# Performance work log

Hardware: AMD Instinct MI355X
Metric: run time of the kernel (lower is better)

The kernel has to match this reference:

```python
import jax, jax.numpy as jnp
import numpy as np

ALPHA = 0.99  # EMA decay used in ewa_func


def setup_inputs() -> dict:
    key = jax.random.key(0)
    k1, k2 = jax.random.split(key)
    N, K, D = 65536, 2048, 128  # flattened latents, vq_num, vq_dim
    initrange = 1.0 / D  # matches init_embed uniform_(-1/vq_dim, 1/vq_dim)
    return {
        "Z": jax.random.normal(k1, (N, D), dtype=jnp.float32),
        "dict_val": jax.random.uniform(k2, (K, D), dtype=jnp.float32,
                                       minval=-initrange, maxval=initrange),
        "dict_cnt": jnp.ones((K,), dtype=jnp.float32),
    }


def reference(Z, dict_val, dict_cnt):
    K, D = dict_val.shape
    # pairwise squared L2 dist: ((Z[:,None]-W[None,:])**2).sum(2), computed as
    # ||z||^2 - 2 z.w + ||w||^2 (same math, GEMM-efficient form)
    z2 = jnp.sum(Z * Z, axis=1)                      # [N]
    w2 = jnp.sum(dict_val * dict_val, axis=1)        # [K]
    dist = z2[:, None] - 2.0 * (Z @ dict_val.T) + w2[None, :]  # [N, K]
    i = jnp.argmin(dist, axis=1)                     # [N] assigned codes

    # EMA codebook update, only for clusters that received assignments
    counts = jax.ops.segment_sum(jnp.ones((Z.shape[0],), Z.dtype), i, num_segments=K)  # [K]
    sums = jax.ops.segment_sum(Z, i, num_segments=K)  # [K, D]
    assigned = counts > 0
    c_new = jnp.where(assigned, ALPHA * dict_cnt + (1.0 - ALPHA) * counts, dict_cnt)
    w_new = jnp.where(
        assigned[:, None],
        ALPHA * dict_val + (1.0 - ALPHA) * sums / jnp.maximum(c_new, 1e-12)[:, None],
        dict_val,
    )

    W_j = w_new[i]                                   # [N, D] quantized vectors
    # straight-through estimator: forward = W_j (detached), grad passes to Z
    st_out = Z + jax.lax.stop_gradient(W_j - Z)
    # commit_loss = L2_dist(Z, sg(W_j)).sum(1).mean()
    diff = Z - jax.lax.stop_gradient(W_j)
    commit_loss = jnp.mean(jnp.sum(diff * diff, axis=1))
    return st_out, commit_loss, w_new, c_new
```

## Files before the change

kernel.cpp:

```cpp
#include <hip/hip_runtime.h>
#include <hip/hip_bf16.h>

#define NN 65536
#define KK 2048
#define DD 128

typedef __attribute__((ext_vector_type(8))) _Float16 f16x8;
typedef __attribute__((ext_vector_type(16))) float f32x16;

static __device__ __forceinline__ unsigned encf(float f) {
    unsigned u = __float_as_uint(f);
    return u ^ (((unsigned)((int)u >> 31)) | 0x80000000u);
}

static __device__ __forceinline__ void gll16(const void* g, void* l) {
    __builtin_amdgcn_global_load_lds(
        (const __attribute__((address_space(1))) void*)g,
        (__attribute__((address_space(3))) void*)l, 16, 0, 0);
}

__global__ __launch_bounds__(256) void vq_prep(const float* __restrict__ Wd,
                                               _Float16* __restrict__ Wre,
                                               float* __restrict__ w2)
{
    int tid = threadIdx.x;
    int rl = tid >> 4, c = tid & 15;
    int r = blockIdx.x * 16 + rl;
    const float4* wp = reinterpret_cast<const float4*>(Wd + (size_t)r * DD + c * 8);
    float4 v0 = wp[0], v1 = wp[1];
    float v[8] = {v0.x, v0.y, v0.z, v0.w, v1.x, v1.y, v1.z, v1.w};

    f16x8 hv;
#pragma unroll
    for (int j = 0; j < 8; ++j) hv[j] = (_Float16)(v[j] * 128.0f);

    float p = 0.f;
#pragma unroll
    for (int j = 0; j < 8; ++j) p = fmaf(v[j], v[j], p);
#pragma unroll
    for (int off2 = 1; off2 < 16; off2 <<= 1) p += __shfl_xor(p, off2, 64);

    int t = c >> 1, g = c & 1;
    size_t off = (size_t)(r >> 7) * 16384 + (size_t)((r >> 5) & 3) * 4096
               + t * 512 + g * 256 + (size_t)(r & 31) * 8;
    *reinterpret_cast<f16x8*>(Wre + off) = hv;
    if (c == 0) w2[r] = p;
}

__global__ __launch_bounds__(256, 2) void vq_gemm(const float* __restrict__ Z,
                                                  const _Float16* __restrict__ Wre,
                                                  const float* __restrict__ w2g,
                                                  const float* __restrict__ Wd,
                                                  int* __restrict__ assign,
                                                  float* __restrict__ counts)
{
    int rb  = blockIdx.x;
    int tid = threadIdx.x;
    int wid = tid >> 6, lane = tid & 63;
    int g2 = lane >> 5, l31 = lane & 31;

    __shared__ _Float16 Bs[2][16384];
    __shared__ float W2s[2048];
    __shared__ float2 T2s[128];

#pragma unroll
    for (int j = 0; j < 2; ++j)
        gll16(w2g + j * 1024 + tid * 4, &W2s[j * 1024 + tid * 4]);
#pragma unroll
    for (int j = 0; j < 8; ++j)
        gll16(Wre + j * 2048 + tid * 8, &Bs[0][j * 2048 + tid * 8]);

    const float* zrow = Z + ((size_t)(rb * 128 + wid * 32 + l31)) * DD + g2 * 8;
    f16x8 a[8];
#pragma unroll
    for (int t = 0; t < 8; ++t) {
        float4 u0 = *reinterpret_cast<const float4*>(zrow + t * 16);
        float4 u1 = *reinterpret_cast<const float4*>(zrow + t * 16 + 4);
        f16x8 h;
        h[0] = (_Float16)u0.x; h[1] = (_Float16)u0.y;
        h[2] = (_Float16)u0.z; h[3] = (_Float16)u0.w;
        h[4] = (_Float16)u1.x; h[5] = (_Float16)u1.y;
        h[6] = (_Float16)u1.z; h[7] = (_Float16)u1.w;
        a[t] = h;
    }

    const float INF = __uint_as_float(0x7F800000u);
    float t1[16], t2[16];
#pragma unroll
    for (int s = 0; s < 16; ++s) { t1[s] = INF; t2[s] = INF; }

    const f32x16 zz = {};

    int cur = 0;
#pragma unroll 1
    for (int it = 0; it < 16; ++it) {
        if (it < 15) {
            const _Float16* wb = Wre + (size_t)(it + 1) * 16384;
#pragma unroll
            for (int j = 0; j < 8; ++j)
                gll16(wb + j * 2048 + tid * 8, &Bs[cur ^ 1][j * 2048 + tid * 8]);
            asm volatile("s_waitcnt vmcnt(8)" ::: "memory");
        } else {
            asm volatile("s_waitcnt vmcnt(0)" ::: "memory");
        }
        __builtin_amdgcn_s_barrier();

        float w2v[4];
#pragma unroll
        for (int ct = 0; ct < 4; ++ct) w2v[ct] = W2s[it * 128 + ct * 32 + l31];

        const _Float16* bb = &Bs[cur][g2 * 256 + l31 * 8];
        f32x16 acc[4];
        __builtin_amdgcn_s_setprio(1);
#pragma unroll
        for (int ct = 0; ct < 4; ++ct) {
#pragma unroll
            for (int t = 0; t < 8; ++t) {
                f16x8 b = *reinterpret_cast<const f16x8*>(bb + ct * 4096 + t * 512);
                acc[ct] = __builtin_amdgcn_mfma_f32_32x32x16_f16(
                    a[t], b, (t == 0) ? zz : acc[ct], 0, 0, 0);
            }
        }
        __builtin_amdgcn_s_setprio(0);

#pragma unroll
        for (int ct = 0; ct < 4; ++ct) {
            unsigned ci = (unsigned)(it * 128 + ct * 32 + l31);
#pragma unroll
            for (int r = 0; r < 16; ++r) {
                float d = fmaf(-0.015625f, acc[ct][r], w2v[ct]);
                float df = __uint_as_float((__float_as_uint(d) & 0xFFFFF800u) | ci);
                t2[r] = __builtin_amdgcn_fmed3f(df, t1[r], t2[r]);
                t1[r] = fminf(t1[r], df);
            }
        }

        __builtin_amdgcn_s_barrier();
        cur ^= 1;
    }

#pragma unroll
    for (int s = 0; s < 16; ++s) {
        float v1 = t1[s], v2 = t2[s];
#pragma unroll
        for (int msk = 1; msk < 32; msk <<= 1) {
            float o1 = __shfl_xor(v1, msk, 64);
            float o2 = __shfl_xor(v2, msk, 64);
            float mx = fmaxf(v1, o1);
            v1 = fminf(v1, o1);
            v2 = fminf(fminf(v2, o2), mx);
        }
        if (l31 == 0) {
            int rl = wid * 32 + (s & 3) + 8 * (s >> 2) + 4 * g2;
            T2s[rl] = make_float2(v1, v2);
        }
    }
    __syncthreads();

    if (tid < 128) {
        int row = rb * 128 + tid;
        float2 t2v = T2s[tid];
        unsigned u1 = __float_as_uint(t2v.x);
        unsigned u2 = __float_as_uint(t2v.y);
        int c1 = (int)(u1 & 2047u), c2 = (int)(u2 & 2047u);
        float d1 = __uint_as_float(u1 & 0xFFFFF800u);
        float d2 = __uint_as_float(u2 & 0xFFFFF800u);

        int res = c1;
        if (d2 - d1 <= 1e-3f) {
            int cols[2] = {c1, c2};
            const float4* zp = reinterpret_cast<const float4*>(Z + (size_t)row * DD);
            float s0 = 0.f, s1 = 0.f, s2 = 0.f, s3 = 0.f;
            for (int q = 0; q < 32; ++q) {
                float4 z = zp[q];
                s0 = fmaf(z.x, z.x, s0);
                s1 = fmaf(z.y, z.y, s1);
                s2 = fmaf(z.z, z.z, s2);
                s3 = fmaf(z.w, z.w, s3);
            }
            float z2v = (s0 + s1) + (s2 + s3);
            unsigned long long be = ~0ull;
            for (int i = 0; i < 2; ++i) {
                int k = cols[i];
                const float4* wp = reinterpret_cast<const float4*>(Wd + (size_t)k * DD);
                float a0 = 0.f, a1 = 0.f, a2 = 0.f, a3 = 0.f;
                for (int q = 0; q < 32; ++q) {
                    float4 zq = zp[q];
                    float4 wq = wp[q];
                    a0 = fmaf(zq.x, wq.x, a0);
                    a1 = fmaf(zq.y, wq.y, a1);
                    a2 = fmaf(zq.z, wq.z, a2);
                    a3 = fmaf(zq.w, wq.w, a3);
                }
                float sdot = (a0 + a1) + (a2 + a3);
                float tt = __fsub_rn(z2v, __fmul_rn(2.0f, sdot));
                float dist = __fadd_rn(tt, W2s[k]);
                unsigned long long key =
                    (((unsigned long long)encf(dist)) << 32) | (unsigned)k;
                if (key < be) be = key;
            }
            res = (int)(be & 0xffffffffu);
        }
        assign[row] = res;
        atomicAdd(&counts[res], 1.0f);
    }
}

__global__ __launch_bounds__(256) void vq_scan(const float* __restrict__ counts,
                                               int* __restrict__ start,
                                               int* __restrict__ cursor)
{
    __shared__ int ps[256];
    int tid = threadIdx.x;
    int c[8];
    int tot = 0;
#pragma unroll
    for (int j = 0; j < 8; ++j) { c[j] = (int)counts[tid * 8 + j]; tot += c[j]; }
    ps[tid] = tot;
    __syncthreads();
    for (int off = 1; off < 256; off <<= 1) {
        int v = (tid >= off) ? ps[tid - off] : 0;
        __syncthreads();
        ps[tid] += v;
        __syncthreads();
    }
    int base = ps[tid] - tot;
#pragma unroll
    for (int j = 0; j < 8; ++j) {
        start[tid * 8 + j] = base;
        cursor[tid * 8 + j] = base;
        base += c[j];
    }
}

__global__ __launch_bounds__(256) void vq_permute(const int* __restrict__ assign,
                                                  int* __restrict__ cursor,
                                                  int* __restrict__ order)
{
    int row = blockIdx.x * 256 + threadIdx.x;
    int k = assign[row];
    int pos = atomicAdd(&cursor[k], 1);
    order[pos] = row;
}

__global__ __launch_bounds__(128) void vq_accum_update(const float* __restrict__ Z,
                                                       const float* __restrict__ Wd,
                                                       const float* __restrict__ dict_cnt,
                                                       const float* __restrict__ counts,
                                                       const int* __restrict__ start,
                                                       const int* __restrict__ order,
                                                       float* __restrict__ w_new_out,
                                                       float* __restrict__ c_new_out,
                                                       float* __restrict__ st_out,
                                                       float* __restrict__ bins)
{
    int k = blockIdx.x;
    int d = threadIdx.x;
    int n = (int)counts[k];
    int st = start[k];

    float sum = 0.f, sq = 0.f;
    int i = 0;
    for (; i + 4 <= n; i += 4) {
        int o0 = order[st + i + 0];
        int o1 = order[st + i + 1];
        int o2 = order[st + i + 2];
        int o3 = order[st + i + 3];
        float v0 = Z[(size_t)o0 * DD + d];
        float v1 = Z[(size_t)o1 * DD + d];
        float v2 = Z[(size_t)o2 * DD + d];
        float v3 = Z[(size_t)o3 * DD + d];
        sum += (v0 + v1) + (v2 + v3);
        sq = fmaf(v0, v0, sq);
        sq = fmaf(v1, v1, sq);
        sq = fmaf(v2, v2, sq);
        sq = fmaf(v3, v3, sq);
    }
    for (; i < n; ++i) {
        float v = Z[(size_t)order[st + i] * DD + d];
        sum += v;
        sq = fmaf(v, v, sq);
    }

    float cnt = dict_cnt[k];
    float ck = counts[k];
    bool assigned = n > 0;
    float cn = assigned ? __fadd_rn(__fmul_rn(0.99f, cnt), __fmul_rn(0.01f, ck)) : cnt;
    float w = Wd[(size_t)k * DD + d];
    float wn = w;
    if (assigned) {
        float num = __fmul_rn(0.01f, sum);
        wn = __fadd_rn(__fmul_rn(0.99f, w), num / fmaxf(cn, 1e-12f));
    }
    w_new_out[(size_t)k * DD + d] = wn;
    if (d == 0) c_new_out[k] = cn;

    int j = 0;
    for (; j + 4 <= n; j += 4) {
        int o0 = order[st + j + 0];
        int o1 = order[st + j + 1];
        int o2 = order[st + j + 2];
        int o3 = order[st + j + 3];
        st_out[(size_t)o0 * DD + d] = wn;
        st_out[(size_t)o1 * DD + d] = wn;
        st_out[(size_t)o2 * DD + d] = wn;
        st_out[(size_t)o3 * DD + d] = wn;
    }
    for (; j < n; ++j)
        st_out[(size_t)order[st + j] * DD + d] = wn;

    float p = fmaf(ck, wn * wn, fmaf(-2.0f * wn, sum, sq));
#pragma unroll
    for (int off = 32; off; off >>= 1) p += __shfl_down(p, off, 64);
    __shared__ float sm[2];
    if ((threadIdx.x & 63) == 0) sm[threadIdx.x >> 6] = p;
    __syncthreads();
    if (threadIdx.x == 0) atomicAdd(&bins[(k & 63) * 16], sm[0] + sm[1]);
}

__global__ void vq_finish(const float* __restrict__ bins,
                          float* __restrict__ out_loss)
{
    if (threadIdx.x == 0) {
        float s = 0.f;
        for (int i = 0; i < 64; ++i) s += bins[i * 16];
        out_loss[0] = s * (1.0f / 65536.0f);
    }
}

extern "C" void kernel_launch(void* const* d_in, const int* in_sizes, int n_in,
                              void* d_out, int out_size, void* d_ws, size_t ws_size,
                              hipStream_t stream)
{
    const float* Z        = (const float*)d_in[0];
    const float* Wd       = (const float*)d_in[1];
    const float* dict_cnt = (const float*)d_in[2];

    float* out      = (float*)d_out;
    float* st_out   = out;
    float* out_loss = out + (size_t)NN * DD;
    float* w_new    = out_loss + 1;
    float* c_new    = w_new + (size_t)KK * DD;

    char* ws = (char*)d_ws;
    _Float16* Wre  = (_Float16*)ws;
    float* w2      = (float*)(ws + 524288);
    int* assign    = (int*)(ws + 532480);
    float* counts  = (float*)(ws + 794624);
    float* bins    = (float*)(ws + 802816);
    int* start     = (int*)(ws + 806912);
    int* cursor    = (int*)(ws + 815104);
    int* order     = (int*)(ws + 823296);

    hipMemsetAsync(counts, 0, 8192 + 4096, stream);

    vq_prep<<<KK / 16, 256, 0, stream>>>(Wd, Wre, w2);
    vq_gemm<<<NN / 128, 256, 0, stream>>>(Z, Wre, w2, Wd, assign, counts);
    vq_scan<<<1, 256, 0, stream>>>(counts, start, cursor);
    vq_permute<<<NN / 256, 256, 0, stream>>>(assign, cursor, order);
    vq_accum_update<<<KK, 128, 0, stream>>>(Z, Wd, dict_cnt, counts, start, order,
                                            w_new, c_new, st_out, bins);
    vq_finish<<<1, 64, 0, stream>>>(bins, out_loss);
}
```

Before: 106.4 us.

## Double GEMM block rows per workgroup and move st_out writes to a coalesced gather

The distance GEMM block grows to 512 threads and 256 rows, so each staged codebook tile in LDS is reused by twice as many rows and per-thread load issues are halved. The scattered per-cluster st_out writes in the accumulate kernel are removed. A separate fully coalesced gather kernel now writes st_out from assign and w_new, and it also takes over the loss finalization. The gather adds a kernel launch and re-reads w_new, and the larger blocks with a 4-block occupancy target may increase register pressure.

```diff
diff --git a/kernel.cpp b/kernel.cpp
--- a/kernel.cpp
+++ b/kernel.cpp
@@ -47,7 +47,7 @@
     if (c == 0) w2[r] = p;
 }
 
-__global__ __launch_bounds__(256, 2) void vq_gemm(const float* __restrict__ Z,
+__global__ __launch_bounds__(512, 4) void vq_gemm(const float* __restrict__ Z,
                                                   const _Float16* __restrict__ Wre,
                                                   const float* __restrict__ w2g,
                                                   const float* __restrict__ Wd,
@@ -61,16 +61,14 @@
 
     __shared__ _Float16 Bs[2][16384];
     __shared__ float W2s[2048];
-    __shared__ float2 T2s[128];
-
-#pragma unroll
-    for (int j = 0; j < 2; ++j)
-        gll16(w2g + j * 1024 + tid * 4, &W2s[j * 1024 + tid * 4]);
-#pragma unroll
-    for (int j = 0; j < 8; ++j)
-        gll16(Wre + j * 2048 + tid * 8, &Bs[0][j * 2048 + tid * 8]);
-
-    const float* zrow = Z + ((size_t)(rb * 128 + wid * 32 + l31)) * DD + g2 * 8;
+    __shared__ float2 T2s[256];
+
+    gll16(w2g + tid * 4, &W2s[tid * 4]);
+#pragma unroll
+    for (int j = 0; j < 4; ++j)
+        gll16(Wre + j * 4096 + tid * 8, &Bs[0][j * 4096 + tid * 8]);
+
+    const float* zrow = Z + ((size_t)(rb * 256 + wid * 32 + l31)) * DD + g2 * 8;
     f16x8 a[8];
 #pragma unroll
     for (int t = 0; t < 8; ++t) {
@@ -97,9 +95,9 @@
         if (it < 15) {
             const _Float16* wb = Wre + (size_t)(it + 1) * 16384;
 #pragma unroll
-            for (int j = 0; j < 8; ++j)
-                gll16(wb + j * 2048 + tid * 8, &Bs[cur ^ 1][j * 2048 + tid * 8]);
-            asm volatile("s_waitcnt vmcnt(8)" ::: "memory");
+            for (int j = 0; j < 4; ++j)
+                gll16(wb + j * 4096 + tid * 8, &Bs[cur ^ 1][j * 4096 + tid * 8]);
+            asm volatile("s_waitcnt vmcnt(4)" ::: "memory");
         } else {
             asm volatile("s_waitcnt vmcnt(0)" ::: "memory");
         }
@@ -157,8 +155,8 @@
     }
     __syncthreads();
 
-    if (tid < 128) {
-        int row = rb * 128 + tid;
+    if (tid < 256) {
+        int row = rb * 256 + tid;
         float2 t2v = T2s[tid];
         unsigned u1 = __float_as_uint(t2v.x);
         unsigned u2 = __float_as_uint(t2v.y);
@@ -251,7 +249,6 @@
                                                        const int* __restrict__ order,
                                                        float* __restrict__ w_new_out,
                                                        float* __restrict__ c_new_out,
-                                                       float* __restrict__ st_out,
                                                        float* __restrict__ bins)
 {
     int k = blockIdx.x;
@@ -295,20 +292,6 @@
     w_new_out[(size_t)k * DD + d] = wn;
     if (d == 0) c_new_out[k] = cn;
 
-    int j = 0;
-    for (; j + 4 <= n; j += 4) {
-        int o0 = order[st + j + 0];
-        int o1 = order[st + j + 1];
-        int o2 = order[st + j + 2];
-        int o3 = order[st + j + 3];
-        st_out[(size_t)o0 * DD + d] = wn;
-        st_out[(size_t)o1 * DD + d] = wn;
-        st_out[(size_t)o2 * DD + d] = wn;
-        st_out[(size_t)o3 * DD + d] = wn;
-    }
-    for (; j < n; ++j)
-        st_out[(size_t)order[st + j] * DD + d] = wn;
-
     float p = fmaf(ck, wn * wn, fmaf(-2.0f * wn, sum, sq));
 #pragma unroll
     for (int off = 32; off; off >>= 1) p += __shfl_down(p, off, 64);
@@ -318,10 +301,18 @@
     if (threadIdx.x == 0) atomicAdd(&bins[(k & 63) * 16], sm[0] + sm[1]);
 }
 
-__global__ void vq_finish(const float* __restrict__ bins,
-                          float* __restrict__ out_loss)
-{
-    if (threadIdx.x == 0) {
+__global__ __launch_bounds__(256) void vq_gather(const int* __restrict__ assign,
+                                                 const float* __restrict__ w_new,
+                                                 float* __restrict__ st_out,
+                                                 const float* __restrict__ bins,
+                                                 float* __restrict__ out_loss)
+{
+    int t = blockIdx.x * 256 + threadIdx.x;
+    int row = t >> 7, d = t & 127;
+    int k = assign[row];
+    st_out[t] = w_new[(size_t)k * DD + d];
+
+    if (blockIdx.x == 0 && threadIdx.x == 0) {
         float s = 0.f;
         for (int i = 0; i < 64; ++i) s += bins[i * 16];
         out_loss[0] = s * (1.0f / 65536.0f);
@@ -355,10 +346,10 @@
     hipMemsetAsync(counts, 0, 8192 + 4096, stream);
 
     vq_prep<<<KK / 16, 256, 0, stream>>>(Wd, Wre, w2);
-    vq_gemm<<<NN / 128, 256, 0, stream>>>(Z, Wre, w2, Wd, assign, counts);
+    vq_gemm<<<NN / 256, 512, 0, stream>>>(Z, Wre, w2, Wd, assign, counts);
     vq_scan<<<1, 256, 0, stream>>>(counts, start, cursor);
     vq_permute<<<NN / 256, 256, 0, stream>>>(assign, cursor, order);
     vq_accum_update<<<KK, 128, 0, stream>>>(Z, Wd, dict_cnt, counts, start, order,
-                                            w_new, c_new, st_out, bins);
-    vq_finish<<<1, 64, 0, stream>>>(bins, out_loss);
-}
+                                            w_new, c_new, bins);
+    vq_gather<<<(NN * DD) / 256, 256, 0, stream>>>(assign, w_new, st_out, bins, out_loss);
+}
```

Measured after the change: 147.3 us. 1.38x slower.
